# Kernel tuning notes

Hardware: AMD Instinct MI355X
Metric: run time of the kernel (lower is better)

The kernel has to match this reference:

```python
import jax, jax.numpy as jnp
import numpy as np

N, DX, DS, NLAB, NSMAT = 20000, 16, 64, 10, 64
E_HALF = 160000
E = 2 * E_HALF
N_LABELED = 2000
N_HIDDEN = 6  # six Linear(nsmat,nsmat) layers between input and output layers


def setup_inputs() -> dict:
    key = jax.random.key(0)
    ks = jax.random.split(key, 16)
    xembed = jax.random.normal(ks[0], (N, DX), jnp.float32)
    sembed = jax.random.normal(ks[1], (N, DS), jnp.float32)
    # ylprob are log-probabilities (original uses exp(ylprob) in the KL term)
    ylprob = jax.nn.log_softmax(jax.random.normal(ks[2], (N, NLAB), jnp.float32), axis=1)
    # build edge list with explicit reverse pairs so loss_orth is exercised
    s_half = jax.random.randint(ks[3], (E_HALF,), 0, N, jnp.int32)
    t_half = jax.random.randint(ks[4], (E_HALF,), 0, N, jnp.int32)
    src = jnp.concatenate([s_half, t_half])
    tgt = jnp.concatenate([t_half, s_half])
    edge_w = jax.random.uniform(ks[5], (E,), jnp.float32, 0.1, 1.0)
    rev1 = jnp.arange(E_HALF, dtype=jnp.int32)
    rev2 = rev1 + E_HALF
    idvert = jax.random.randint(ks[6], (N_LABELED,), 0, N, jnp.int32)
    fcW_in = jax.random.normal(ks[7], (2 * DS, NSMAT), jnp.float32) / np.sqrt(2 * DS)
    fcb_in = jnp.zeros((NSMAT,), jnp.float32)
    fcW_h = jax.random.normal(ks[8], (N_HIDDEN, NSMAT, NSMAT), jnp.float32) / np.sqrt(NSMAT)
    fcb_h = jnp.zeros((N_HIDDEN, NSMAT), jnp.float32)
    fcW_out = jax.random.normal(ks[9], (NSMAT, DX * DX), jnp.float32) / np.sqrt(NSMAT)
    fcb_out = jnp.zeros((DX * DX,), jnp.float32)
    # cl_smat params: Linear(dimx, nlab) + LogSoftmax
    clW = jax.random.normal(ks[10], (DX, NLAB), jnp.float32) / np.sqrt(DX)
    clb = jnp.zeros((NLAB,), jnp.float32)
    return dict(xembed=xembed, sembed=sembed, ylprob=ylprob, edge_w=edge_w,
                fcW_in=fcW_in, fcb_in=fcb_in, fcW_h=fcW_h, fcb_h=fcb_h,
                fcW_out=fcW_out, fcb_out=fcb_out, clW=clW, clb=clb,
                src=src, tgt=tgt, rev1=rev1, rev2=rev2, idvert=idvert)


def _edge_matrices(sf, tf, fcW_in, fcb_in, fcW_h, fcb_h, fcW_out, fcb_out):
    # [E, 2*dims] -> 8-layer ReLU MLP -> [E, dimx, dimx]
    h = jax.nn.relu(jnp.concatenate([sf, tf], axis=1) @ fcW_in + fcb_in)
    for i in range(N_HIDDEN):
        h = jax.nn.relu(h @ fcW_h[i] + fcb_h[i])
    return (h @ fcW_out + fcb_out).reshape(-1, DX, DX)


def reference(xembed, sembed, ylprob, edge_w, fcW_in, fcb_in, fcW_h, fcb_h,
              fcW_out, fcb_out, clW, clb, src, tgt, rev1, rev2, idvert):
    # per-edge sheaf transport matrices from gathered structure embeddings
    edge_mats = _edge_matrices(sembed[src], sembed[tgt],
                               fcW_in, fcb_in, fcW_h, fcb_h, fcW_out, fcb_out)

    # orthogonality loss over reverse edge pairs: mean RMS(A@B - I) * dimx
    prod = jnp.einsum('eij,ejk->eik', edge_mats[rev1], edge_mats[rev2])
    diff = prod - jnp.eye(DX, dtype=prod.dtype)
    loss_orth = jnp.mean(jnp.sqrt(jnp.mean(diff * diff, axis=(1, 2)) * (DX * DX)))

    # message passing: gather -> bmm -> weighted scatter-add -> degree normalize
    messages = jnp.einsum('eij,ej->ei', edge_mats, xembed[src])  # [E, dimx]
    weighted = messages * edge_w[:, None]
    new_x = jax.ops.segment_sum(weighted, tgt, num_segments=N)   # [N, dimx]
    deg = jax.ops.segment_sum(edge_w, tgt, num_segments=N)       # [N]
    xmaped = jnp.where((deg > 0)[:, None], new_x / jnp.maximum(deg, 1e-20)[:, None], new_x)

    loss_smap = jnp.mean((xmaped - xembed) ** 2) * DX

    # KL(y || g) on labeled nodes; cl_smat = Linear + LogSoftmax
    glprob = jax.nn.log_softmax(xmaped[idvert] @ clW + clb, axis=1)
    ylp = ylprob[idvert]
    loss_lbpr = jnp.mean(jnp.sum(jnp.exp(ylp) * (ylp - glprob), axis=1))

    # original recomputes the same MLP on the same inputs and takes the MSE of
    # two identical tensors -> exactly zero (and zero gradient)
    loss_cons = jnp.zeros((), xembed.dtype)

    return (loss_orth, loss_cons, loss_smap, loss_lbpr)
```

## Files before the change

### kernel.cpp

```cpp
#include <hip/hip_runtime.h>
#include <hip/hip_bf16.h>

#define N_NODES   20000
#define DX        16
#define DS        64
#define NLAB      10
#define NSMAT     64
#define E_HALF    160000
#define E_TOT     320000
#define N_LABELED 2000
#define N_HIDDEN  6

#define PAIRS 32
#define NT    (E_HALF / PAIRS)

typedef short bf16x8 __attribute__((ext_vector_type(8)));
typedef float f32x4  __attribute__((ext_vector_type(4)));
#define MFMA16(a, b, c) __builtin_amdgcn_mfma_f32_16x16x32_bf16((a), (b), (c), 0, 0, 0)

#define LDS_A0    0
#define LDS_H0    16384
#define LDS_H1    24576
#define LDS_MT    16384
#define LDS_TOTAL 32768

#define SWZ(row)  ((((row) & 7) << 4) ^ (((row) & 8) << 2))
#define CSP(c)    (((c) & 12) << 2)

#define WS_W0     0
#define WS_WH     16384
#define WS_WOUT   65536
#define WS_FLOATS 98304

__device__ __forceinline__ unsigned short f2bf(float f) {
    unsigned int u = __float_as_uint(f);
    unsigned int r = (u + 0x7fffu + ((u >> 16) & 1u)) >> 16;
    return (unsigned short)r;
}
__device__ __forceinline__ unsigned int cvtpk(float lo, float hi) {
    unsigned int r;
    asm("v_cvt_pk_bf16_f32 %0, %1, %2" : "=v"(r) : "v"(lo), "v"(hi));
    return r;
}
__device__ __forceinline__ float bflo(unsigned int u) { return __uint_as_float(u << 16); }
__device__ __forceinline__ float bfhi(unsigned int u) { return __uint_as_float(u & 0xffff0000u); }

__global__ void k_prep(const float* __restrict__ Win, const float* __restrict__ Wh,
                       const float* __restrict__ Wout, unsigned short* __restrict__ wsw) {
    const int idx = blockIdx.x * 256 + threadIdx.x;
    if (idx >= 49152) return;
    float val; int base, KK, k, n;
    if (idx < 8192) {
        k = idx >> 6; n = idx & 63; val = Win[idx]; base = WS_W0 / 2; KK = 4;
    } else if (idx < 32768) {
        const int r = idx - 8192; const int l = r >> 12; const int rr = r & 4095;
        k = rr >> 6; n = rr & 63; val = Wh[r]; base = (WS_WH + l * 8192) / 2; KK = 2;
    } else {
        const int r = idx - 32768; k = r >> 8; n = r & 255;
        val = Wout[r]; base = WS_WOUT / 2; KK = 2;
    }
    const int ntile = n >> 4, kk = k >> 5, hi = (k >> 3) & 3, j = k & 7;
    const int lane = hi * 16 + (n & 15);
    wsw[base + (((ntile * KK + kk) * 64 + lane) * 8 + j)] = f2bf(val);
}

__global__ void k_zero(float* __restrict__ p, int n) {
    int i = blockIdx.x * blockDim.x + threadIdx.x;
    const int stride = gridDim.x * blockDim.x;
    for (; i < n; i += stride) p[i] = 0.0f;
}

__global__ __launch_bounds__(256, 5) void k_main(
    const float* __restrict__ xembed, const float* __restrict__ sembed,
    const float* __restrict__ edge_w,
    const float* __restrict__ bin, const float* __restrict__ bh,
    const float* __restrict__ bout,
    const int* __restrict__ src, const int* __restrict__ tgt,
    const unsigned short* __restrict__ wsw,
    float* __restrict__ newx, float* __restrict__ deg,
    float* __restrict__ orth_part)
{
    extern __shared__ char lds[];
    const int tid    = threadIdx.x;
    const int lane   = tid & 63;
    const int wv     = tid >> 6;
    const int lane15 = lane & 15;
    const int hi     = lane >> 4;
    const int p0     = blockIdx.x * PAIRS;

    float4 sx;
    {
        const int si = tid >> 3, sc = tid & 7;
        const bool sT = (sc >= 4); const int scc = sc & 3;
        const int p = p0 + si;
        const int nodeA = sT ? tgt[p] : src[p];
        const float4* nrow = (const float4*)(sembed + (size_t)nodeA * DS + scc * 16);
        const float4 v0 = nrow[0], v1 = nrow[1], v2 = nrow[2], v3 = nrow[3];
        const int colA = (sT ? 128 : 0) + scc * 32;
        const int colB = (sT ? 0 : 128) + scc * 32;
        const int sXor = SWZ(si);
        uint2 pk;
        pk.x = cvtpk(v0.x, v0.y); pk.y = cvtpk(v0.z, v0.w);
        *(uint2*)(lds + LDS_A0 + si * 256 + ((colA + 0) ^ sXor)) = pk;
        *(uint2*)(lds + LDS_A0 + (32 + si) * 256 + ((colB + 0) ^ sXor)) = pk;
        pk.x = cvtpk(v1.x, v1.y); pk.y = cvtpk(v1.z, v1.w);
        *(uint2*)(lds + LDS_A0 + si * 256 + ((colA + 8) ^ sXor)) = pk;
        *(uint2*)(lds + LDS_A0 + (32 + si) * 256 + ((colB + 8) ^ sXor)) = pk;
        pk.x = cvtpk(v2.x, v2.y); pk.y = cvtpk(v2.z, v2.w);
        *(uint2*)(lds + LDS_A0 + si * 256 + ((colA + 16) ^ sXor)) = pk;
        *(uint2*)(lds + LDS_A0 + (32 + si) * 256 + ((colB + 16) ^ sXor)) = pk;
        pk.x = cvtpk(v3.x, v3.y); pk.y = cvtpk(v3.z, v3.w);
        *(uint2*)(lds + LDS_A0 + si * 256 + ((colA + 24) ^ sXor)) = pk;
        *(uint2*)(lds + LDS_A0 + (32 + si) * 256 + ((colB + 24) ^ sXor)) = pk;

        const int sed = tid >> 2, sqq = tid & 3;
        const int nodeX = (sed < 32) ? src[p0 + sed] : tgt[p0 + sed - 32];
        sx = *(const float4*)(xembed + (size_t)nodeX * DX + sqq * 4);
    }

    float bin_r[4];
    #pragma unroll
    for (int n = 0; n < 4; ++n) bin_r[n] = bin[16 * n + lane15];

    const int arow = 16 * wv + lane15;
    const int axor = SWZ(arow);

    __syncthreads();

    {
        bf16x8 a[4];
        #pragma unroll
        for (int kk = 0; kk < 4; ++kk)
            a[kk] = *(const bf16x8*)(lds + LDS_A0 + arow * 256 + ((kk * 64 + hi * 16) ^ axor));
        const unsigned short* w0g = wsw + WS_W0 / 2;
        #pragma unroll
        for (int n = 0; n < 4; ++n) {
            f32x4 acc = {0.0f, 0.0f, 0.0f, 0.0f};
            #pragma unroll
            for (int kk = 0; kk < 4; ++kk) {
                const bf16x8 b = *(const bf16x8*)(w0g + ((n * 4 + kk) * 64 + lane) * 8);
                acc = MFMA16(a[kk], b, acc);
            }
            #pragma unroll
            for (int r = 0; r < 4; ++r) {
                const int row = 16 * wv + 4 * hi + r;
                *(__hip_bfloat16*)(lds + LDS_H0 + row * 128 +
                    (((16 * n + lane15) * 2) ^ SWZ(row))) =
                    __float2bfloat16(fmaxf(acc[r] + bin_r[n], 0.0f));
            }
        }
    }
    __syncthreads();

    float bcur[4], bnxt[4];
    {
        const float* bl = bh + lane15;
        bcur[0] = bl[0]; bcur[1] = bl[16]; bcur[2] = bl[32]; bcur[3] = bl[48];
    }
    #pragma unroll
    for (int l = 0; l < N_HIDDEN; ++l) {
        if (l + 1 < N_HIDDEN) {
            const float* bl = bh + (l + 1) * 64 + lane15;
            bnxt[0] = bl[0]; bnxt[1] = bl[16]; bnxt[2] = bl[32]; bnxt[3] = bl[48];
        }
        const int sB = (l & 1) ? LDS_H1 : LDS_H0;
        const int dB = (l & 1) ? LDS_H0 : LDS_H1;
        const unsigned short* whg = wsw + WS_WH / 2 + l * 4096;
        const bf16x8 a0 = *(const bf16x8*)(lds + sB + arow * 128 + ((hi * 16) ^ axor));
        const bf16x8 a1 = *(const bf16x8*)(lds + sB + arow * 128 + ((64 + hi * 16) ^ axor));
        #pragma unroll
        for (int n = 0; n < 4; ++n) {
            f32x4 acc = {0.0f, 0.0f, 0.0f, 0.0f};
            const bf16x8 b0 = *(const bf16x8*)(whg + ((n * 2 + 0) * 64 + lane) * 8);
            const bf16x8 b1 = *(const bf16x8*)(whg + ((n * 2 + 1) * 64 + lane) * 8);
            acc = MFMA16(a0, b0, acc);
            acc = MFMA16(a1, b1, acc);
            #pragma unroll
            for (int r = 0; r < 4; ++r) {
                const int row = 16 * wv + 4 * hi + r;
                *(__hip_bfloat16*)(lds + dB + row * 128 +
                    (((16 * n + lane15) * 2) ^ SWZ(row))) =
                    __float2bfloat16(fmaxf(acc[r] + bcur[n], 0.0f));
            }
        }
        bcur[0] = bnxt[0]; bcur[1] = bnxt[1]; bcur[2] = bnxt[2]; bcur[3] = bnxt[3];
    }

    const bf16x8 fa0 = *(const bf16x8*)(lds + LDS_H0 + arow * 128 + ((hi * 16) ^ axor));
    const bf16x8 fa1 = *(const bf16x8*)(lds + LDS_H0 + arow * 128 + ((64 + hi * 16) ^ axor));
    __syncthreads();

    {
        float bo[16];
        #pragma unroll
        for (int n = 0; n < 16; ++n) bo[n] = bout[16 * n + lane15];

        const unsigned short* wog = wsw + WS_WOUT / 2;
        if (wv < 2) {
            #pragma unroll
            for (int n = 0; n < 16; ++n) {
                const bf16x8 b0 = *(const bf16x8*)(wog + ((n * 2 + 0) * 64 + lane) * 8);
                const bf16x8 b1 = *(const bf16x8*)(wog + ((n * 2 + 1) * 64 + lane) * 8);
                f32x4 acc = {0.0f, 0.0f, 0.0f, 0.0f};
                acc = MFMA16(fa0, b0, acc);
                acc = MFMA16(fa1, b1, acc);
                #pragma unroll
                for (int r = 0; r < 4; ++r) {
                    const int i = 16 * wv + 4 * hi + r;
                    *(__hip_bfloat16*)(lds + LDS_A0 + i * 512 +
                        (((n * 16 + lane15) * 2) ^ SWZ(i))) =
                        __float2bfloat16(acc[r] + bo[n]);
                }
            }
        } else {
            unsigned int pk0[8], pk1[8], pk2[8], pk3[8];
            float tmp0 = 0.f, tmp1 = 0.f, tmp2 = 0.f, tmp3 = 0.f;
            #pragma unroll
            for (int n = 0; n < 16; ++n) {
                const bf16x8 b0 = *(const bf16x8*)(wog + ((n * 2 + 0) * 64 + lane) * 8);
                const bf16x8 b1 = *(const bf16x8*)(wog + ((n * 2 + 1) * 64 + lane) * 8);
                f32x4 acc = {0.0f, 0.0f, 0.0f, 0.0f};
                acc = MFMA16(fa0, b0, acc);
                acc = MFMA16(fa1, b1, acc);
                const float v0 = acc[0] + bo[n], v1 = acc[1] + bo[n];
                const float v2 = acc[2] + bo[n], v3 = acc[3] + bo[n];
                if (n & 1) {
                    pk0[n >> 1] = cvtpk(tmp0, v0); pk1[n >> 1] = cvtpk(tmp1, v1);
                    pk2[n >> 1] = cvtpk(tmp2, v2); pk3[n >> 1] = cvtpk(tmp3, v3);
                } else {
                    tmp0 = v0; tmp1 = v1; tmp2 = v2; tmp3 = v3;
                }
            }
            const int csp = CSP(lane15);
            #pragma unroll
            for (int r = 0; r < 4; ++r) {
                const int i = 16 * (wv - 2) + 4 * hi + r;
                const int sw = SWZ(i) ^ csp;
                char* base = lds + LDS_MT + i * 512;
                const unsigned int* pkr = (r == 0) ? pk0 : (r == 1) ? pk1 : (r == 2) ? pk2 : pk3;
                *(uint4*)(base + ((lane15 * 32 + 0) ^ sw)) =
                    make_uint4(pkr[0], pkr[1], pkr[2], pkr[3]);
                *(uint4*)(base + ((lane15 * 32 + 16) ^ sw)) =
                    make_uint4(pkr[4], pkr[5], pkr[6], pkr[7]);
            }
        }
    }
    __syncthreads();

    {
        const int e = tid >> 2, q = tid & 3;
        const int i = e & 31;
        const bool isB = (e >= 32);
        float xv[16];
        #pragma unroll
        for (int qq = 0; qq < 4; ++qq) {
            xv[4 * qq + 0] = __shfl(sx.x, qq, 4);
            xv[4 * qq + 1] = __shfl(sx.y, qq, 4);
            xv[4 * qq + 2] = __shfl(sx.z, qq, 4);
            xv[4 * qq + 3] = __shfl(sx.w, qq, 4);
        }
        const int p = p0 + i;
        const float w_e  = isB ? edge_w[p + E_HALF] : edge_w[p];
        const int target = isB ? src[p] : tgt[p];
        const int ixor = SWZ(i);
        if (!isB) {
            #pragma unroll
            for (int jj = 0; jj < 4; ++jj) {
                const int row = 4 * q + jj;
                const uint4 m0 = *(const uint4*)(lds + LDS_A0 + i * 512 + ((row * 32) ^ ixor));
                const uint4 m1 = *(const uint4*)(lds + LDS_A0 + i * 512 + ((row * 32 + 16) ^ ixor));
                float m = bflo(m0.x) * xv[0];
                m = fmaf(bfhi(m0.x), xv[1], m);  m = fmaf(bflo(m0.y), xv[2], m);
                m = fmaf(bfhi(m0.y), xv[3], m);  m = fmaf(bflo(m0.z), xv[4], m);
                m = fmaf(bfhi(m0.z), xv[5], m);  m = fmaf(bflo(m0.w), xv[6], m);
                m = fmaf(bfhi(m0.w), xv[7], m);  m = fmaf(bflo(m1.x), xv[8], m);
                m = fmaf(bfhi(m1.x), xv[9], m);  m = fmaf(bflo(m1.y), xv[10], m);
                m = fmaf(bfhi(m1.y), xv[11], m); m = fmaf(bflo(m1.z), xv[12], m);
                m = fmaf(bfhi(m1.z), xv[13], m); m = fmaf(bflo(m1.w), xv[14], m);
                m = fmaf(bfhi(m1.w), xv[15], m);
                atomicAdd(&newx[(size_t)target * DX + row], w_e * m);
            }
        } else {
            float macc[4] = {0.f, 0.f, 0.f, 0.f};
            #pragma unroll
            for (int c = 0; c < 16; ++c) {
                const uint2 v = *(const uint2*)(lds + LDS_MT + i * 512 +
                                                ((c * 32 + q * 8) ^ ixor ^ CSP(c)));
                const float xc = xv[c];
                macc[0] = fmaf(bflo(v.x), xc, macc[0]);
                macc[1] = fmaf(bfhi(v.x), xc, macc[1]);
                macc[2] = fmaf(bflo(v.y), xc, macc[2]);
                macc[3] = fmaf(bfhi(v.y), xc, macc[3]);
            }
            #pragma unroll
            for (int jj = 0; jj < 4; ++jj)
                atomicAdd(&newx[(size_t)target * DX + 4 * q + jj], w_e * macc[jj]);
        }
        if (q == 0) atomicAdd(&deg[target], w_e);
    }

    float wsum = 0.0f;
    {
        const bf16x8 zf = {0, 0, 0, 0, 0, 0, 0, 0};
        #pragma unroll
        for (int pp = 0; pp < 8; ++pp) {
            const int pi = 8 * wv + pp;
            const int pxor = SWZ(pi);
            const int offA = (lane15 * 32 + (hi & 1) * 16) ^ pxor;
            const int offB = (lane15 * 32 + (hi & 1) * 16) ^ pxor ^ CSP(lane15);
            bf16x8 af  = *(const bf16x8*)(lds + LDS_A0 + pi * 512 + offA);
            bf16x8 bfr = *(const bf16x8*)(lds + LDS_MT + pi * 512 + offB);
            if (hi >= 2) { af = zf; bfr = zf; }
            f32x4 pr = {0.f, 0.f, 0.f, 0.f};
            pr = MFMA16(af, bfr, pr);
            float ss = 0.0f;
            #pragma unroll
            for (int r = 0; r < 4; ++r) {
                const float d = pr[r] - ((4 * hi + r == lane15) ? 1.0f : 0.0f);
                ss = fmaf(d, d, ss);
            }
            #pragma unroll
            for (int o = 32; o > 0; o >>= 1) ss += __shfl_xor(ss, o, 64);
            wsum += sqrtf(ss);
        }
    }
    __syncthreads();
    if (lane == 0) ((float*)(lds + LDS_A0))[wv] = wsum;
    __syncthreads();
    if (tid == 0) {
        const float* pw = (const float*)(lds + LDS_A0);
        atomicAdd(&orth_part[blockIdx.x & 255], pw[0] + pw[1] + pw[2] + pw[3]);
    }
}

__device__ __forceinline__ float block_reduce_256(float v) {
    __shared__ float part[4];
    #pragma unroll
    for (int off = 32; off > 0; off >>= 1) v += __shfl_xor(v, off, 64);
    const int lane = threadIdx.x & 63, wid = threadIdx.x >> 6;
    if (lane == 0) part[wid] = v;
    __syncthreads();
    float s = 0.0f;
    if (threadIdx.x == 0) {
        #pragma unroll
        for (int i = 0; i < 4; ++i) s += part[i];
    }
    return s;
}

__global__ __launch_bounds__(256) void k_smap(
    const float* __restrict__ xembed, float* __restrict__ nx,
    const float* __restrict__ deg, float* __restrict__ accum)
{
    const int n = blockIdx.x * 256 + threadIdx.x;
    float ss = 0.0f;
    if (n < N_NODES) {
        const float d = deg[n];
        const float inv = 1.0f / fmaxf(d, 1e-20f);
        #pragma unroll
        for (int c = 0; c < DX; ++c) {
            const float v  = nx[(size_t)n * DX + c];
            const float xm = (d > 0.0f) ? v * inv : v;
            nx[(size_t)n * DX + c] = xm;
            const float df = xm - xembed[(size_t)n * DX + c];
            ss = fmaf(df, df, ss);
        }
    }
    ss = block_reduce_256(ss);
    if (threadIdx.x == 0) atomicAdd(&accum[1], ss);
}

__global__ __launch_bounds__(256) void k_lbpr(
    const float* __restrict__ ylprob, const float* __restrict__ xmaped,
    const float* __restrict__ clW, const float* __restrict__ clb,
    const int* __restrict__ idvert, float* __restrict__ accum)
{
    const int v = blockIdx.x * 256 + threadIdx.x;
    float kl = 0.0f;
    if (v < N_LABELED) {
        const int n = idvert[v];
        float z[NLAB];
        #pragma unroll
        for (int c = 0; c < NLAB; ++c) z[c] = clb[c];
        #pragma unroll
        for (int i = 0; i < DX; ++i) {
            const float xi = xmaped[(size_t)n * DX + i];
            #pragma unroll
            for (int c = 0; c < NLAB; ++c) z[c] = fmaf(xi, clW[i * NLAB + c], z[c]);
        }
        float mx = z[0];
        #pragma unroll
        for (int c = 1; c < NLAB; ++c) mx = fmaxf(mx, z[c]);
        float se = 0.0f;
        #pragma unroll
        for (int c = 0; c < NLAB; ++c) se += expf(z[c] - mx);
        const float lse = mx + logf(se);
        #pragma unroll
        for (int c = 0; c < NLAB; ++c) {
            const float yl = ylprob[(size_t)n * NLAB + c];
            kl += expf(yl) * (yl - (z[c] - lse));
        }
    }
    kl = block_reduce_256(kl);
    if (threadIdx.x == 0) atomicAdd(&accum[2], kl);
}

__global__ __launch_bounds__(256) void k_final(
    const float* __restrict__ accum, const float* __restrict__ orth_part,
    float* __restrict__ out)
{
    float v = orth_part[threadIdx.x];
    v = block_reduce_256(v);
    if (threadIdx.x == 0) {
        out[0] = v * (1.0f / (float)E_HALF);
        out[1] = 0.0f;
        out[2] = accum[1] * (1.0f / (float)N_NODES);
        out[3] = accum[2] * (1.0f / (float)N_LABELED);
    }
}

extern "C" void kernel_launch(void* const* d_in, const int* in_sizes, int n_in,
                              void* d_out, int out_size, void* d_ws, size_t ws_size,
                              hipStream_t stream) {
    const float* xembed = (const float*)d_in[0];
    const float* sembed = (const float*)d_in[1];
    const float* ylprob = (const float*)d_in[2];
    const float* edge_w = (const float*)d_in[3];
    const float* Win    = (const float*)d_in[4];
    const float* bin    = (const float*)d_in[5];
    const float* Wh     = (const float*)d_in[6];
    const float* bh     = (const float*)d_in[7];
    const float* Wout   = (const float*)d_in[8];
    const float* bout   = (const float*)d_in[9];
    const float* clW    = (const float*)d_in[10];
    const float* clb    = (const float*)d_in[11];
    const int*   src    = (const int*)d_in[12];
    const int*   tgt    = (const int*)d_in[13];
    const int*   idvert = (const int*)d_in[16];

    unsigned short* wsw = (unsigned short*)d_ws;
    float* wsF       = (float*)((char*)d_ws + WS_FLOATS);
    float* newx      = wsF;
    float* deg       = wsF + (size_t)N_NODES * DX;
    float* accum     = deg + N_NODES;
    float* orth_part = accum + 4;
    const int nzero = N_NODES * DX + N_NODES + 4 + 256;

    k_prep<<<192, 256, 0, stream>>>(Win, Wh, Wout, wsw);
    k_zero<<<512, 256, 0, stream>>>(wsF, nzero);

    k_main<<<NT, 256, LDS_TOTAL, stream>>>(
        xembed, sembed, edge_w, bin, bh, bout, src, tgt, wsw, newx, deg, orth_part);

    k_smap<<<(N_NODES + 255) / 256, 256, 0, stream>>>(xembed, newx, deg, accum);
    k_lbpr<<<(N_LABELED + 255) / 256, 256, 0, stream>>>(ylprob, newx, clW, clb, idvert, accum);
    k_final<<<1, 256, 0, stream>>>(accum, orth_part, (float*)d_out);
}
```

Baseline: 156.7 us.

## Prefetch MLP weights into registers and relocate output-matrix LDS region

Hidden-layer weight fragments are now loaded into registers one layer ahead, and output-layer weight fragments are software-pipelined four tiles deep, so global weight loads overlap MFMA work. The LDS region for the transposed matrix moves to a new offset and total LDS grows, which lets the sync after the first layer be removed and the final activation read move after the barrier. Occupancy bound drops from 5 to 4 blocks to allow the extra registers. This risks lower occupancy and more register pressure.

```diff
diff --git a/kernel.cpp b/kernel.cpp
--- a/kernel.cpp
+++ b/kernel.cpp
@@ -21,8 +21,8 @@
 #define LDS_A0    0
 #define LDS_H0    16384
 #define LDS_H1    24576
-#define LDS_MT    16384
-#define LDS_TOTAL 32768
+#define LDS_MT    24576
+#define LDS_TOTAL 40960
 
 #define SWZ(row)  ((((row) & 7) << 4) ^ (((row) & 8) << 2))
 #define CSP(c)    (((c) & 12) << 2)
@@ -70,7 +70,7 @@
     for (; i < n; i += stride) p[i] = 0.0f;
 }
 
-__global__ __launch_bounds__(256, 5) void k_main(
+__global__ __launch_bounds__(256, 4) void k_main(
     const float* __restrict__ xembed, const float* __restrict__ sembed,
     const float* __restrict__ edge_w,
     const float* __restrict__ bin, const float* __restrict__ bh,
@@ -125,6 +125,14 @@
     const int arow = 16 * wv + lane15;
     const int axor = SWZ(arow);
 
+    bf16x8 wcur[8], wnxt[8];
+    {
+        const unsigned short* whg = wsw + WS_WH / 2;
+        #pragma unroll
+        for (int j = 0; j < 8; ++j)
+            wcur[j] = *(const bf16x8*)(whg + (j * 64 + lane) * 8);
+    }
+
     __syncthreads();
 
     {
@@ -150,7 +158,6 @@
             }
         }
     }
-    __syncthreads();
 
     float bcur[4], bnxt[4];
     {
@@ -160,21 +167,22 @@
     #pragma unroll
     for (int l = 0; l < N_HIDDEN; ++l) {
         if (l + 1 < N_HIDDEN) {
+            const unsigned short* whg = wsw + WS_WH / 2 + (l + 1) * 4096;
+            #pragma unroll
+            for (int j = 0; j < 8; ++j)
+                wnxt[j] = *(const bf16x8*)(whg + (j * 64 + lane) * 8);
             const float* bl = bh + (l + 1) * 64 + lane15;
             bnxt[0] = bl[0]; bnxt[1] = bl[16]; bnxt[2] = bl[32]; bnxt[3] = bl[48];
         }
         const int sB = (l & 1) ? LDS_H1 : LDS_H0;
         const int dB = (l & 1) ? LDS_H0 : LDS_H1;
-        const unsigned short* whg = wsw + WS_WH / 2 + l * 4096;
         const bf16x8 a0 = *(const bf16x8*)(lds + sB + arow * 128 + ((hi * 16) ^ axor));
         const bf16x8 a1 = *(const bf16x8*)(lds + sB + arow * 128 + ((64 + hi * 16) ^ axor));
         #pragma unroll
         for (int n = 0; n < 4; ++n) {
             f32x4 acc = {0.0f, 0.0f, 0.0f, 0.0f};
-            const bf16x8 b0 = *(const bf16x8*)(whg + ((n * 2 + 0) * 64 + lane) * 8);
-            const bf16x8 b1 = *(const bf16x8*)(whg + ((n * 2 + 1) * 64 + lane) * 8);
-            acc = MFMA16(a0, b0, acc);
-            acc = MFMA16(a1, b1, acc);
+            acc = MFMA16(a0, wcur[2 * n + 0], acc);
+            acc = MFMA16(a1, wcur[2 * n + 1], acc);
             #pragma unroll
             for (int r = 0; r < 4; ++r) {
                 const int row = 16 * wv + 4 * hi + r;
@@ -183,11 +191,10 @@
                     __float2bfloat16(fmaxf(acc[r] + bcur[n], 0.0f));
             }
         }
+        #pragma unroll
+        for (int j = 0; j < 8; ++j) wcur[j] = wnxt[j];
         bcur[0] = bnxt[0]; bcur[1] = bnxt[1]; bcur[2] = bnxt[2]; bcur[3] = bnxt[3];
     }
-
-    const bf16x8 fa0 = *(const bf16x8*)(lds + LDS_H0 + arow * 128 + ((hi * 16) ^ axor));
-    const bf16x8 fa1 = *(const bf16x8*)(lds + LDS_H0 + arow * 128 + ((64 + hi * 16) ^ axor));
     __syncthreads();
 
     {
@@ -195,12 +202,25 @@
         #pragma unroll
         for (int n = 0; n < 16; ++n) bo[n] = bout[16 * n + lane15];
 
+        const bf16x8 fa0 = *(const bf16x8*)(lds + LDS_H0 + arow * 128 + ((hi * 16) ^ axor));
+        const bf16x8 fa1 = *(const bf16x8*)(lds + LDS_H0 + arow * 128 + ((64 + hi * 16) ^ axor));
         const unsigned short* wog = wsw + WS_WOUT / 2;
+
+        bf16x8 pbA[4], pbB[4];
+        #pragma unroll
+        for (int n = 0; n < 4; ++n) {
+            pbA[n] = *(const bf16x8*)(wog + ((n * 2 + 0) * 64 + lane) * 8);
+            pbB[n] = *(const bf16x8*)(wog + ((n * 2 + 1) * 64 + lane) * 8);
+        }
+
         if (wv < 2) {
             #pragma unroll
             for (int n = 0; n < 16; ++n) {
-                const bf16x8 b0 = *(const bf16x8*)(wog + ((n * 2 + 0) * 64 + lane) * 8);
-                const bf16x8 b1 = *(const bf16x8*)(wog + ((n * 2 + 1) * 64 + lane) * 8);
+                const bf16x8 b0 = pbA[n & 3], b1 = pbB[n & 3];
+                if (n + 4 < 16) {
+                    pbA[n & 3] = *(const bf16x8*)(wog + (((n + 4) * 2 + 0) * 64 + lane) * 8);
+                    pbB[n & 3] = *(const bf16x8*)(wog + (((n + 4) * 2 + 1) * 64 + lane) * 8);
+                }
                 f32x4 acc = {0.0f, 0.0f, 0.0f, 0.0f};
                 acc = MFMA16(fa0, b0, acc);
                 acc = MFMA16(fa1, b1, acc);
@@ -217,8 +237,11 @@
             float tmp0 = 0.f, tmp1 = 0.f, tmp2 = 0.f, tmp3 = 0.f;
             #pragma unroll
             for (int n = 0; n < 16; ++n) {
-                const bf16x8 b0 = *(const bf16x8*)(wog + ((n * 2 + 0) * 64 + lane) * 8);
-                const bf16x8 b1 = *(const bf16x8*)(wog + ((n * 2 + 1) * 64 + lane) * 8);
+                const bf16x8 b0 = pbA[n & 3], b1 = pbB[n & 3];
+                if (n + 4 < 16) {
+                    pbA[n & 3] = *(const bf16x8*)(wog + (((n + 4) * 2 + 0) * 64 + lane) * 8);
+                    pbB[n & 3] = *(const bf16x8*)(wog + (((n + 4) * 2 + 1) * 64 + lane) * 8);
+                }
                 f32x4 acc = {0.0f, 0.0f, 0.0f, 0.0f};
                 acc = MFMA16(fa0, b0, acc);
                 acc = MFMA16(fa1, b1, acc);
```

New measurement: 129.6 us (median of 2 runs). 1.21x faster.
